# Kernel optimization log

Hardware: AMD Instinct MI355X
Metric: run time of the kernel (lower is better)

The kernel has to match this reference:

```python
import jax, jax.numpy as jnp
import numpy as np

NUM_HEADS = 8
EPS = 1e-12  # torch F.normalize eps


def _l2norm(t):
    # F.normalize(t, dim=-1): t / max(||t||, eps)
    n = jnp.sqrt(jnp.sum(t * t, axis=-1, keepdims=True))
    return t / jnp.maximum(n, EPS)


def setup_inputs() -> dict:
    key = jax.random.key(0)
    ks = jax.random.split(key, 4)
    B, C, H, W = 16, 384, 32, 32
    x = jax.random.normal(ks[0], (B, C, H, W), dtype=jnp.float32)
    temperature = jnp.ones((NUM_HEADS, 1, 1), dtype=jnp.float32)
    qkv_w = jax.random.normal(ks[1], (3 * C, C), dtype=jnp.float32) * (1.0 / np.sqrt(C))
    qkv_b = jnp.zeros((3 * C,), dtype=jnp.float32)
    proj_w = jax.random.normal(ks[2], (C, C), dtype=jnp.float32) * (1.0 / np.sqrt(C))
    proj_b = jnp.zeros((C,), dtype=jnp.float32)
    return {"x": x, "temperature": temperature, "qkv_w": qkv_w,
            "qkv_b": qkv_b, "proj_w": proj_w, "proj_b": proj_b}


def reference(x, temperature, qkv_w, qkv_b, proj_w, proj_b):
    B, C, H, W = x.shape
    nH = NUM_HEADS
    hd = C // nH
    N = H * W
    x_flat = x.reshape(B, C, N).transpose(0, 2, 1)            # [B, N, C]
    qkv = x_flat @ qkv_w.T + qkv_b                             # [B, N, 3C]
    qkv = qkv.reshape(B, N, 3, nH, hd).transpose(2, 0, 3, 1, 4)  # [3, B, nH, N, hd]
    q, k, v = qkv[0], qkv[1], qkv[2]
    q = _l2norm(q)
    k = _l2norm(k)
    attn = jnp.einsum('bhnd,bhmd->bhnm', q, k) * temperature   # [B, nH, N, N]
    attn = jax.nn.softmax(attn, axis=-1)
    out = jnp.einsum('bhnm,bhmd->bhnd', attn, v)               # [B, nH, N, hd]
    out = out.transpose(0, 2, 1, 3).reshape(B, N, C)           # [B, N, C]
    out = out @ proj_w.T + proj_b
    return out.transpose(0, 2, 1).reshape(B, C, H, W)
```

## Files before the change

### kernel.cpp

```cpp
#include <hip/hip_runtime.h>
#include <hip/hip_bf16.h>

#define Bb   16
#define Cc   384
#define Nn   1024
#define NH   8
#define HD   48
#define C3   1152
#define D64  64
#define KTS  72
#define PSTR 72

typedef _Float16 f16x8 __attribute__((ext_vector_type(8)));
typedef float    f32x4 __attribute__((ext_vector_type(4)));
typedef unsigned short ushort8 __attribute__((ext_vector_type(8)));

__device__ inline unsigned short f2h(float f) {
  union { _Float16 h; unsigned short u; } cv;
  cv.h = (_Float16)f;
  return cv.u;
}
__device__ inline float h2f(unsigned short s) {
  union { _Float16 h; unsigned short u; } cv;
  cv.u = s;
  return (float)cv.h;
}
__device__ inline unsigned int packh(float a, float b) {
  return (unsigned int)f2h(a) | ((unsigned int)f2h(b) << 16);
}

__device__ inline void gload_lds16(const unsigned short* g, unsigned short* l) {
  __builtin_amdgcn_global_load_lds(
      (const __attribute__((address_space(1))) void*)g,
      (__attribute__((address_space(3))) void*)l, 16, 0, 0);
}

__global__ __launch_bounds__(256) void prep_kernel(
    const float* __restrict__ qkv_w, const float* __restrict__ pw,
    unsigned short* __restrict__ wqh, unsigned short* __restrict__ pwh,
    unsigned short* __restrict__ vt) {
  const int bid = blockIdx.x;
  if (bid < 1728) {
    int i = bid * 256 + threadIdx.x;
    wqh[i] = f2h(qkv_w[i]);
  } else if (bid < 2304) {
    int i = (bid - 1728) * 256 + threadIdx.x;
    pwh[i] = f2h(pw[i]);
  } else {
    int idx8 = (bid - 2304) * 256 + threadIdx.x;
    int bh = idx8 >> 11;
    int rem = idx8 & 2047;
    int row = 48 + (rem >> 7);
    int col = (rem & 127) * 8;
    unsigned short fill = (row == 48) ? (unsigned short)0x3C00 : (unsigned short)0;
    ushort8 v;
#pragma unroll
    for (int j = 0; j < 8; j++) v[j] = fill;
    *(ushort8*)(vt + (size_t)bh * D64 * Nn + (size_t)row * Nn + col) = v;
  }
}

__global__ __launch_bounds__(256) void xsplit_kernel(
    const float* __restrict__ x, unsigned short* __restrict__ xh) {
  __shared__ float tile[64][65];
  const int b  = blockIdx.z;
  const int c0 = blockIdx.y * 64;
  const int n0 = blockIdx.x * 64;
  const int t  = threadIdx.x;
  const int rl = t >> 2, sc = (t & 3) * 16;
  {
    const float* src = x + ((size_t)b * Cc + c0 + rl) * Nn + n0 + sc;
#pragma unroll
    for (int i = 0; i < 4; i++) {
      float4 v = *(const float4*)(src + i * 4);
      tile[rl][sc + i * 4 + 0] = v.x; tile[rl][sc + i * 4 + 1] = v.y;
      tile[rl][sc + i * 4 + 2] = v.z; tile[rl][sc + i * 4 + 3] = v.w;
    }
  }
  __syncthreads();
  {
    ushort8 h0, h1;
#pragma unroll
    for (int i = 0; i < 8; i++) h0[i] = f2h(tile[sc + i][rl]);
#pragma unroll
    for (int i = 0; i < 8; i++) h1[i] = f2h(tile[sc + 8 + i][rl]);
    size_t dst = ((size_t)b * Nn + n0 + rl) * Cc + c0 + sc;
    *(ushort8*)(xh + dst) = h0; *(ushort8*)(xh + dst + 8) = h1;
  }
}

__global__ __launch_bounds__(256, 4) void qkv_mfma(
    const unsigned short* __restrict__ wh,
    const unsigned short* __restrict__ xh,
    const float* __restrict__ bias,
    unsigned short* __restrict__ qh, unsigned short* __restrict__ kh,
    unsigned short* __restrict__ vt) {
  __shared__ unsigned short lds[128 * 136];
  unsigned short* Ash = lds;
  unsigned short* Bsh = lds + 6144;

  const int b  = blockIdx.z;
  const int yb = blockIdx.y;
  const int j0 = yb * 96;
  const int n0 = blockIdx.x * 128;
  const int tid = threadIdx.x;
  const int wave = tid >> 6, lane = tid & 63;
  const int quad = lane >> 4, l16 = lane & 15;
  const int wm = (wave >> 1) * 48, wn = (wave & 1) * 64;
  const int hs = wave >> 1;

  f32x4 acc[3][4];
#pragma unroll
  for (int mi = 0; mi < 3; mi++)
#pragma unroll
    for (int ni = 0; ni < 4; ni++) acc[mi][ni] = (f32x4){0.f, 0.f, 0.f, 0.f};

  const int sw = l16 & 7;

  for (int c0 = 0; c0 < Cc; c0 += 64) {
    __syncthreads();
#pragma unroll
    for (int s = 0; s < 3; s++) {
      int r  = s * 32 + wave * 8 + (lane >> 3);
      int cg = ((lane & 7) ^ (lane >> 3)) * 8;
      gload_lds16(wh + (size_t)(j0 + r) * Cc + c0 + cg,
                  &Ash[(s * 32 + wave * 8) * 64]);
    }
#pragma unroll
    for (int s = 0; s < 4; s++) {
      int r  = s * 32 + wave * 8 + (lane >> 3);
      int cg = ((lane & 7) ^ (lane >> 3)) * 8;
      gload_lds16(xh + ((size_t)b * Nn + n0 + r) * Cc + c0 + cg,
                  &Bsh[(s * 32 + wave * 8) * 64]);
    }
    __syncthreads();

#pragma unroll
    for (int ks = 0; ks < 64; ks += 32) {
      const int ach = (((ks >> 3) + quad) ^ sw) * 8;
      f16x8 ah[3], bh[4];
#pragma unroll
      for (int mi = 0; mi < 3; mi++)
        ah[mi] = *(const f16x8*)&Ash[(wm + mi * 16 + l16) * 64 + ach];
#pragma unroll
      for (int ni = 0; ni < 4; ni++)
        bh[ni] = *(const f16x8*)&Bsh[(wn + ni * 16 + l16) * 64 + ach];
#pragma unroll
      for (int mi = 0; mi < 3; mi++)
#pragma unroll
        for (int ni = 0; ni < 4; ni++)
          acc[mi][ni] = __builtin_amdgcn_mfma_f32_16x16x32_f16(ah[mi], bh[ni], acc[mi][ni], 0, 0, 0);
    }
  }

  const int part = yb >> 2;
  const int tq   = yb & 3;
  float bv[3][4];
#pragma unroll
  for (int mi = 0; mi < 3; mi++)
#pragma unroll
    for (int r = 0; r < 4; r++)
      bv[mi][r] = bias[j0 + wm + mi * 16 + quad * 4 + r];

  if (part < 2) {
    unsigned short* dst = part ? kh : qh;
    __syncthreads();
#pragma unroll
    for (int ni = 0; ni < 4; ni++) {
      float vals[3][4];
      float ss = 0.f;
#pragma unroll
      for (int mi = 0; mi < 3; mi++)
#pragma unroll
        for (int r = 0; r < 4; r++) {
          float v = acc[mi][ni][r] + bv[mi][r];
          vals[mi][r] = v; ss += v * v;
        }
      ss += __shfl_xor(ss, 16);
      ss += __shfl_xor(ss, 32);
      float scale = 1.0f / fmaxf(sqrtf(ss), 1e-12f);
      int n = wn + ni * 16 + l16;
#pragma unroll
      for (int mi = 0; mi < 3; mi++) {
        ushort4 sv;
        sv.x = f2h(vals[mi][0] * scale);
        sv.y = f2h(vals[mi][1] * scale);
        sv.z = f2h(vals[mi][2] * scale);
        sv.w = f2h(vals[mi][3] * scale);
        *(ushort4*)&lds[n * 136 + hs * 64 + mi * 16 + quad * 4] = sv;
      }
    }
    {
      int n = tid >> 1, h2 = tid & 1;
      ushort8 z = {0, 0, 0, 0, 0, 0, 0, 0};
      *(ushort8*)&lds[n * 136 + h2 * 64 + 48] = z;
      *(ushort8*)&lds[n * 136 + h2 * 64 + 56] = z;
    }
    __syncthreads();
#pragma unroll
    for (int it = 0; it < 8; it++) {
      int n = wave * 32 + it * 4 + (lane >> 4);
      int chunk = lane & 15;
      int hs3 = chunk >> 3, c8 = (chunk & 7) * 8;
      int h = 2 * tq + hs3;
      ushort8 v = *(const ushort8*)&lds[n * 136 + hs3 * 64 + c8];
      *(ushort8*)(dst + ((size_t)(b * NH + h) * Nn + n0 + n) * D64 + c8) = v;
    }
  } else {
    const int h = 2 * tq + hs;
#pragma unroll
    for (int mi = 0; mi < 3; mi++) {
#pragma unroll
      for (int r = 0; r < 4; r++) {
        int d = mi * 16 + quad * 4 + r;
        unsigned short* vrow = vt + ((size_t)(b * NH + h) * D64 + d) * Nn;
#pragma unroll
        for (int ni = 0; ni < 4; ni++) {
          int n = n0 + wn + ni * 16 + l16;
          vrow[n] = f2h(acc[mi][ni][r] + bv[mi][r]);
        }
      }
    }
  }
}

__global__ __launch_bounds__(256, 4) void attn_mfma(
    const unsigned short* __restrict__ qh, const unsigned short* __restrict__ kh,
    const unsigned short* __restrict__ vt, const float* __restrict__ temp,
    unsigned short* __restrict__ obh) {
  __shared__ unsigned short Kt[64 * KTS];
  __shared__ unsigned short Vt[64 * KTS];
  __shared__ unsigned short Pt[4 * 32 * PSTR];

  const int bid = blockIdx.x;
  const int hb = bid & 127;
  const int q0 = (bid >> 7) * 128;
  const int b = hb >> 3, h = hb & 7;
  const int tid = threadIdx.x;
  const int wave = tid >> 6, lane = tid & 63;
  const int quad = lane >> 4, l16 = lane & 15;

  const size_t headQ = ((size_t)(b * NH + h) * Nn) * D64;
  const unsigned short* Qg = qh + headQ + (size_t)(q0 + wave * 32) * D64;
  const unsigned short* Kg = kh + headQ;
  const unsigned short* Vg = vt + ((size_t)(b * NH + h) * D64) * Nn;

  f16x8 qa0[2], qa1[2];
#pragma unroll
  for (int m = 0; m < 2; m++) {
    qa0[m] = *(const f16x8*)(Qg + (m * 16 + l16) * D64 + quad * 8);
    qa1[m] = *(const f16x8*)(Qg + (m * 16 + l16) * D64 + quad * 8 + 32);
  }

  const float T2 = temp[h] * 1.44269504f;
  const float M2 = fabsf(T2);

  f32x4 oacc[2][4];
#pragma unroll
  for (int m = 0; m < 2; m++)
#pragma unroll
    for (int g = 0; g < 4; g++) oacc[m][g] = (f32x4){0.f, 0.f, 0.f, 0.f};
  const f32x4 zf = (f32x4){0.f, 0.f, 0.f, 0.f};

  unsigned short* Ptw = Pt + wave * 32 * PSTR;
  const int skey = tid >> 2;
  const int spart = (tid & 3) * 16;

  const unsigned short* ksrc = Kg + (size_t)skey * D64 + spart;
  const unsigned short* vsrc = Vg + (size_t)skey * Nn + spart;
  unsigned short* kdst = Kt + skey * KTS + spart;
  unsigned short* vdst = Vt + skey * KTS + spart;

  uint4 kr0 = *(const uint4*)(ksrc);
  uint4 kr1 = *(const uint4*)(ksrc + 8);
  uint4 vr0 = *(const uint4*)(vsrc);
  uint4 vr1 = *(const uint4*)(vsrc + 8);

  for (int kt = 0; kt < Nn / 64; kt++) {
    __syncthreads();
    *(uint4*)kdst = kr0;
    *(uint4*)(kdst + 8) = kr1;
    *(uint4*)vdst = vr0;
    *(uint4*)(vdst + 8) = vr1;
    __syncthreads();

    if (kt < Nn / 64 - 1) {
      const unsigned short* kn = ksrc + (size_t)(kt + 1) * 64 * D64;
      const unsigned short* vn = vsrc + (size_t)(kt + 1) * 64;
      kr0 = *(const uint4*)kn;
      kr1 = *(const uint4*)(kn + 8);
      vr0 = *(const uint4*)vn;
      vr1 = *(const uint4*)(vn + 8);
    }

    f32x4 sT[2][4];
#pragma unroll
    for (int g = 0; g < 4; g++) {
      const unsigned short* kb = Kt + (g * 16 + l16) * KTS + quad * 8;
      f16x8 kf0 = *(const f16x8*)kb;
      f16x8 kf1 = *(const f16x8*)(kb + 32);
#pragma unroll
      for (int m = 0; m < 2; m++) {
        f32x4 s = __builtin_amdgcn_mfma_f32_16x16x32_f16(kf0, qa0[m], zf, 0, 0, 0);
        sT[m][g] = __builtin_amdgcn_mfma_f32_16x16x32_f16(kf1, qa1[m], s, 0, 0, 0);
      }
    }

#pragma unroll
    for (int m = 0; m < 2; m++) {
#pragma unroll
      for (int g = 0; g < 4; g++) {
        uint2 pw;
        pw.x = packh(__builtin_amdgcn_exp2f(sT[m][g][0] * T2 - M2),
                     __builtin_amdgcn_exp2f(sT[m][g][1] * T2 - M2));
        pw.y = packh(__builtin_amdgcn_exp2f(sT[m][g][2] * T2 - M2),
                     __builtin_amdgcn_exp2f(sT[m][g][3] * T2 - M2));
        *(uint2*)(Ptw + (m * 16 + l16) * PSTR + g * 16 + quad * 4) = pw;
      }
    }

    f16x8 pa[2][2];
#pragma unroll
    for (int m = 0; m < 2; m++) {
      pa[m][0] = *(const f16x8*)(Ptw + (m * 16 + l16) * PSTR + quad * 8);
      pa[m][1] = *(const f16x8*)(Ptw + (m * 16 + l16) * PSTR + quad * 8 + 32);
    }

#pragma unroll
    for (int g = 0; g < 4; g++) {
      const unsigned short* vb0 = Vt + (g * 16 + l16) * KTS + quad * 8;
      f16x8 vf0 = *(const f16x8*)vb0;
      f16x8 vf1 = *(const f16x8*)(vb0 + 32);
#pragma unroll
      for (int m = 0; m < 2; m++) {
        oacc[m][g] = __builtin_amdgcn_mfma_f32_16x16x32_f16(vf0, pa[m][0], oacc[m][g], 0, 0, 0);
        oacc[m][g] = __builtin_amdgcn_mfma_f32_16x16x32_f16(vf1, pa[m][1], oacc[m][g], 0, 0, 0);
      }
    }
  }

#pragma unroll
  for (int m = 0; m < 2; m++) {
    float inv = 1.0f / __shfl(oacc[m][3][0], l16);
    size_t obase = ((size_t)b * Nn + q0 + wave * 32 + m * 16 + l16) * Cc + h * HD;
#pragma unroll
    for (int g = 0; g < 3; g++) {
      ushort4 sv;
      sv.x = f2h(oacc[m][g][0] * inv);
      sv.y = f2h(oacc[m][g][1] * inv);
      sv.z = f2h(oacc[m][g][2] * inv);
      sv.w = f2h(oacc[m][g][3] * inv);
      *(ushort4*)(obh + obase + g * 16 + quad * 4) = sv;
    }
  }
}

__global__ __launch_bounds__(256, 4) void proj_mfma(
    const unsigned short* __restrict__ pwh,
    const unsigned short* __restrict__ obh,
    const float* __restrict__ pb, float* __restrict__ out) {
  __shared__ unsigned short Ash[128 * 64];
  __shared__ unsigned short Bsh[128 * 64];
  const int b  = blockIdx.z;
  const int c0m = blockIdx.y * 128;
  const int n0 = blockIdx.x * 128;
  const int tid = threadIdx.x;
  const int wave = tid >> 6, lane = tid & 63;
  const int quad = lane >> 4, l16 = lane & 15;
  const int wm = (wave >> 1) * 64, wn = (wave & 1) * 64;

  f32x4 acc[4][4];
#pragma unroll
  for (int mi = 0; mi < 4; mi++)
#pragma unroll
    for (int ni = 0; ni < 4; ni++) acc[mi][ni] = (f32x4){0.f, 0.f, 0.f, 0.f};

  const int sw = l16 & 7;

  for (int j0 = 0; j0 < Cc; j0 += 64) {
    __syncthreads();
#pragma unroll
    for (int s = 0; s < 4; s++) {
      int r  = s * 32 + wave * 8 + (lane >> 3);
      int cg = ((lane & 7) ^ (lane >> 3)) * 8;
      gload_lds16(pwh + (size_t)(c0m + r) * Cc + j0 + cg,
                  &Ash[(s * 32 + wave * 8) * 64]);
      gload_lds16(obh + ((size_t)b * Nn + n0 + r) * Cc + j0 + cg,
                  &Bsh[(s * 32 + wave * 8) * 64]);
    }
    __syncthreads();

#pragma unroll
    for (int ks = 0; ks < 64; ks += 32) {
      const int ach = (((ks >> 3) + quad) ^ sw) * 8;
      f16x8 ah[4], bh[4];
#pragma unroll
      for (int mi = 0; mi < 4; mi++)
        ah[mi] = *(const f16x8*)&Ash[(wm + mi * 16 + l16) * 64 + ach];
#pragma unroll
      for (int ni = 0; ni < 4; ni++)
        bh[ni] = *(const f16x8*)&Bsh[(wn + ni * 16 + l16) * 64 + ach];
#pragma unroll
      for (int mi = 0; mi < 4; mi++)
#pragma unroll
        for (int ni = 0; ni < 4; ni++)
          acc[mi][ni] = __builtin_amdgcn_mfma_f32_16x16x32_f16(ah[mi], bh[ni], acc[mi][ni], 0, 0, 0);
    }
  }

#pragma unroll
  for (int mi = 0; mi < 4; mi++) {
#pragma unroll
    for (int r = 0; r < 4; r++) {
      int c = c0m + wm + mi * 16 + quad * 4 + r;
      float bvv = pb[c];
#pragma unroll
      for (int ni = 0; ni < 4; ni++) {
        int n = n0 + wn + ni * 16 + l16;
        out[((size_t)b * Cc + c) * Nn + n] = acc[mi][ni][r] + bvv;
      }
    }
  }
}

extern "C" void kernel_launch(void* const* d_in, const int* in_sizes, int n_in,
                              void* d_out, int out_size, void* d_ws, size_t ws_size,
                              hipStream_t stream) {
  const float* x     = (const float*)d_in[0];
  const float* temp  = (const float*)d_in[1];
  const float* qkv_w = (const float*)d_in[2];
  const float* qkv_b = (const float*)d_in[3];
  const float* pw    = (const float*)d_in[4];
  const float* pb    = (const float*)d_in[5];
  float* out = (float*)d_out;

  const size_t QKN = (size_t)Bb * NH * Nn * D64;
  const size_t WQN = (size_t)C3 * Cc;
  const size_t PWN = (size_t)Cc * Cc;

  unsigned short* Qh  = (unsigned short*)d_ws;
  unsigned short* Kh  = Qh + QKN;
  unsigned short* VhT = Kh + QKN;
  unsigned short* Wqh = VhT + QKN;
  unsigned short* Pwh = Wqh + WQN;
  unsigned short* Xth = Pwh + PWN;
  unsigned short* Obh = Xth;

  prep_kernel<<<3328, 256, 0, stream>>>(qkv_w, pw, Wqh, Pwh, VhT);
  xsplit_kernel<<<dim3(Nn / 64, Cc / 64, Bb), 256, 0, stream>>>(x, Xth);
  qkv_mfma<<<dim3(Nn / 128, C3 / 96, Bb), 256, 0, stream>>>(Wqh, Xth, qkv_b, Qh, Kh, VhT);
  attn_mfma<<<1024, 256, 0, stream>>>(Qh, Kh, VhT, temp, Obh);
  proj_mfma<<<dim3(Nn / 128, Cc / 128, Bb), 256, 0, stream>>>(Pwh, Obh, pb, out);
}
```

Before: 167.4 us.

## Double-buffer K/V via direct-to-LDS loads, swizzle LDS, keep P in registers

The attention kernel now streams K and V tiles straight into double-buffered LDS using global_load_lds, with an XOR swizzle replacing the padded layout. This removes the register staging and one of the two barriers per tile. The softmax probability tile no longer round-trips through LDS: it is packed with cvt_pkrtz and rearranged across lanes with v_permlane16_swap, and the V reads use a matching permuted k-order. The final divide becomes a fast reciprocal. In exchange the kernel relies on gfx950-specific permlane swap semantics and gets round-toward-zero fp16 conversion of P. The barrier logic is also subtle, since the next tile's direct loads must complete before it is read after a single sync.

```diff
diff --git a/kernel.cpp b/kernel.cpp
--- a/kernel.cpp
+++ b/kernel.cpp
@@ -8,10 +8,9 @@
 #define HD   48
 #define C3   1152
 #define D64  64
-#define KTS  72
-#define PSTR 72
 
 typedef _Float16 f16x8 __attribute__((ext_vector_type(8)));
+typedef __fp16   h16x2 __attribute__((ext_vector_type(2)));
 typedef float    f32x4 __attribute__((ext_vector_type(4)));
 typedef unsigned short ushort8 __attribute__((ext_vector_type(8)));
 
@@ -20,13 +19,19 @@
   cv.h = (_Float16)f;
   return cv.u;
 }
-__device__ inline float h2f(unsigned short s) {
-  union { _Float16 h; unsigned short u; } cv;
-  cv.u = s;
-  return (float)cv.h;
-}
-__device__ inline unsigned int packh(float a, float b) {
-  return (unsigned int)f2h(a) | ((unsigned int)f2h(b) << 16);
+__device__ inline unsigned int pk2u(float a, float b) {
+  union { h16x2 v; unsigned int u; } cv;
+  cv.v = __builtin_amdgcn_cvt_pkrtz(a, b);
+  return cv.u;
+}
+__device__ inline void plswap(unsigned int &a, unsigned int &b) {
+  asm("v_permlane16_swap_b32 %0, %1" : "+v"(a), "+v"(b));
+}
+__device__ inline f16x8 mk8(unsigned int a, unsigned int b,
+                            unsigned int c, unsigned int d) {
+  union { unsigned int u[4]; f16x8 h; } cv;
+  cv.u[0] = a; cv.u[1] = b; cv.u[2] = c; cv.u[3] = d;
+  return cv.h;
 }
 
 __device__ inline void gload_lds16(const unsigned short* g, unsigned short* l) {
@@ -228,9 +233,8 @@
     const unsigned short* __restrict__ qh, const unsigned short* __restrict__ kh,
     const unsigned short* __restrict__ vt, const float* __restrict__ temp,
     unsigned short* __restrict__ obh) {
-  __shared__ unsigned short Kt[64 * KTS];
-  __shared__ unsigned short Vt[64 * KTS];
-  __shared__ unsigned short Pt[4 * 32 * PSTR];
+  __shared__ __align__(16) unsigned short Kt[2][64 * 64];
+  __shared__ __align__(16) unsigned short Vt[2][64 * 64];
 
   const int bid = blockIdx.x;
   const int hb = bid & 127;
@@ -239,6 +243,8 @@
   const int tid = threadIdx.x;
   const int wave = tid >> 6, lane = tid & 63;
   const int quad = lane >> 4, l16 = lane & 15;
+  const int qsw = ((quad & 1) << 1) | (quad >> 1);
+  const int sx = (l16 & 7) * 8;
 
   const size_t headQ = ((size_t)(b * NH + h) * Nn) * D64;
   const unsigned short* Qg = qh + headQ + (size_t)(q0 + wave * 32) * D64;
@@ -262,43 +268,38 @@
     for (int g = 0; g < 4; g++) oacc[m][g] = (f32x4){0.f, 0.f, 0.f, 0.f};
   const f32x4 zf = (f32x4){0.f, 0.f, 0.f, 0.f};
 
-  unsigned short* Ptw = Pt + wave * 32 * PSTR;
-  const int skey = tid >> 2;
-  const int spart = (tid & 3) * 16;
-
-  const unsigned short* ksrc = Kg + (size_t)skey * D64 + spart;
-  const unsigned short* vsrc = Vg + (size_t)skey * Nn + spart;
-  unsigned short* kdst = Kt + skey * KTS + spart;
-  unsigned short* vdst = Vt + skey * KTS + spart;
-
-  uint4 kr0 = *(const uint4*)(ksrc);
-  uint4 kr1 = *(const uint4*)(ksrc + 8);
-  uint4 vr0 = *(const uint4*)(vsrc);
-  uint4 vr1 = *(const uint4*)(vsrc + 8);
+  const int srow = lane >> 3;
+  const int scol = ((lane & 7) ^ srow) * 8;
+  const int r0 = wave * 16;
+  const unsigned short* KgS = Kg + (size_t)(r0 + srow) * D64 + scol;
+  const unsigned short* VgS = Vg + (size_t)(r0 + srow) * Nn + scol;
+
+  gload_lds16(KgS,           &Kt[0][r0 * 64]);
+  gload_lds16(KgS + 8 * D64, &Kt[0][(r0 + 8) * 64]);
+  gload_lds16(VgS,           &Vt[0][r0 * 64]);
+  gload_lds16(VgS + 8 * Nn,  &Vt[0][(r0 + 8) * 64]);
 
   for (int kt = 0; kt < Nn / 64; kt++) {
     __syncthreads();
-    *(uint4*)kdst = kr0;
-    *(uint4*)(kdst + 8) = kr1;
-    *(uint4*)vdst = vr0;
-    *(uint4*)(vdst + 8) = vr1;
-    __syncthreads();
-
+    const int cur = kt & 1;
     if (kt < Nn / 64 - 1) {
-      const unsigned short* kn = ksrc + (size_t)(kt + 1) * 64 * D64;
-      const unsigned short* vn = vsrc + (size_t)(kt + 1) * 64;
-      kr0 = *(const uint4*)kn;
-      kr1 = *(const uint4*)(kn + 8);
-      vr0 = *(const uint4*)vn;
-      vr1 = *(const uint4*)(vn + 8);
-    }
+      const unsigned short* kn = KgS + (size_t)(kt + 1) * 64 * D64;
+      const unsigned short* vn = VgS + (size_t)(kt + 1) * 64;
+      gload_lds16(kn,           &Kt[cur ^ 1][r0 * 64]);
+      gload_lds16(kn + 8 * D64, &Kt[cur ^ 1][(r0 + 8) * 64]);
+      gload_lds16(vn,           &Vt[cur ^ 1][r0 * 64]);
+      gload_lds16(vn + 8 * Nn,  &Vt[cur ^ 1][(r0 + 8) * 64]);
+    }
+    const unsigned short* Kl = Kt[cur];
+    const unsigned short* Vl = Vt[cur];
 
     f32x4 sT[2][4];
 #pragma unroll
     for (int g = 0; g < 4; g++) {
-      const unsigned short* kb = Kt + (g * 16 + l16) * KTS + quad * 8;
-      f16x8 kf0 = *(const f16x8*)kb;
-      f16x8 kf1 = *(const f16x8*)(kb + 32);
+      const unsigned short* kb = Kl + (g * 16 + l16) * 64;
+      const int go = (quad * 8) ^ sx;
+      f16x8 kf0 = *(const f16x8*)&kb[go];
+      f16x8 kf1 = *(const f16x8*)&kb[go ^ 32];
 #pragma unroll
       for (int m = 0; m < 2; m++) {
         f32x4 s = __builtin_amdgcn_mfma_f32_16x16x32_f16(kf0, qa0[m], zf, 0, 0, 0);
@@ -306,31 +307,36 @@
       }
     }
 
+    unsigned int w0[2][4], w1[2][4];
+#pragma unroll
+    for (int m = 0; m < 2; m++)
+#pragma unroll
+      for (int g = 0; g < 4; g++) {
+        float e0 = __builtin_amdgcn_exp2f(sT[m][g][0] * T2 - M2);
+        float e1 = __builtin_amdgcn_exp2f(sT[m][g][1] * T2 - M2);
+        float e2 = __builtin_amdgcn_exp2f(sT[m][g][2] * T2 - M2);
+        float e3 = __builtin_amdgcn_exp2f(sT[m][g][3] * T2 - M2);
+        w0[m][g] = pk2u(e0, e1);
+        w1[m][g] = pk2u(e2, e3);
+      }
+
+    f16x8 pa[2][2];
 #pragma unroll
     for (int m = 0; m < 2; m++) {
-#pragma unroll
-      for (int g = 0; g < 4; g++) {
-        uint2 pw;
-        pw.x = packh(__builtin_amdgcn_exp2f(sT[m][g][0] * T2 - M2),
-                     __builtin_amdgcn_exp2f(sT[m][g][1] * T2 - M2));
-        pw.y = packh(__builtin_amdgcn_exp2f(sT[m][g][2] * T2 - M2),
-                     __builtin_amdgcn_exp2f(sT[m][g][3] * T2 - M2));
-        *(uint2*)(Ptw + (m * 16 + l16) * PSTR + g * 16 + quad * 4) = pw;
-      }
-    }
-
-    f16x8 pa[2][2];
-#pragma unroll
-    for (int m = 0; m < 2; m++) {
-      pa[m][0] = *(const f16x8*)(Ptw + (m * 16 + l16) * PSTR + quad * 8);
-      pa[m][1] = *(const f16x8*)(Ptw + (m * 16 + l16) * PSTR + quad * 8 + 32);
+      plswap(w0[m][0], w0[m][1]);
+      plswap(w1[m][0], w1[m][1]);
+      plswap(w0[m][2], w0[m][3]);
+      plswap(w1[m][2], w1[m][3]);
+      pa[m][0] = mk8(w0[m][0], w1[m][0], w0[m][1], w1[m][1]);
+      pa[m][1] = mk8(w0[m][2], w1[m][2], w0[m][3], w1[m][3]);
     }
 
 #pragma unroll
     for (int g = 0; g < 4; g++) {
-      const unsigned short* vb0 = Vt + (g * 16 + l16) * KTS + quad * 8;
-      f16x8 vf0 = *(const f16x8*)vb0;
-      f16x8 vf1 = *(const f16x8*)(vb0 + 32);
+      const unsigned short* vb = Vl + (g * 16 + l16) * 64;
+      const int go = (qsw * 8) ^ sx;
+      f16x8 vf0 = *(const f16x8*)&vb[go];
+      f16x8 vf1 = *(const f16x8*)&vb[go ^ 32];
 #pragma unroll
       for (int m = 0; m < 2; m++) {
         oacc[m][g] = __builtin_amdgcn_mfma_f32_16x16x32_f16(vf0, pa[m][0], oacc[m][g], 0, 0, 0);
@@ -341,7 +347,7 @@
 
 #pragma unroll
   for (int m = 0; m < 2; m++) {
-    float inv = 1.0f / __shfl(oacc[m][3][0], l16);
+    float inv = __builtin_amdgcn_rcpf(__shfl(oacc[m][3][0], l16));
     size_t obase = ((size_t)b * Nn + q0 + wave * 32 + m * 16 + l16) * Cc + h * HD;
 #pragma unroll
     for (int g = 0; g < 3; g++) {
```

Result: faster. 163.7 us (-2.2%).
